# Optimization experiments

Hardware: AMD Instinct MI355X
Metric: run time of the kernel (lower is better)

The kernel has to match this reference:

```python
import math
import jax, jax.numpy as jnp
import numpy as np

NUM_FRAMES = 512
NUM_ANIMALS = 4
N_HEAD = 8
N_EMBD = 512
B = 2
T = NUM_FRAMES * NUM_ANIMALS  # 2048


def _block_causal_mask():
    # tril over frames, full attention within each frame across animals
    tril = jnp.tril(jnp.ones((NUM_FRAMES, NUM_FRAMES), dtype=jnp.float32))
    return jnp.kron(tril, jnp.ones((NUM_ANIMALS, NUM_ANIMALS), dtype=jnp.float32))  # [T, T]


def setup_inputs() -> dict:
    key = jax.random.key(0)
    ks = jax.random.split(key, 6)
    s = 1.0 / math.sqrt(N_EMBD)
    return {
        "x": jax.random.normal(ks[0], (B, T, N_EMBD), dtype=jnp.float32),
        "mask": jnp.ones((B, T), dtype=jnp.int32),
        "Wq": jax.random.normal(ks[1], (N_EMBD, N_EMBD), dtype=jnp.float32) * s,
        "bq": jnp.zeros((N_EMBD,), dtype=jnp.float32),
        "Wk": jax.random.normal(ks[2], (N_EMBD, N_EMBD), dtype=jnp.float32) * s,
        "bk": jnp.zeros((N_EMBD,), dtype=jnp.float32),
        "Wv": jax.random.normal(ks[3], (N_EMBD, N_EMBD), dtype=jnp.float32) * s,
        "bv": jnp.zeros((N_EMBD,), dtype=jnp.float32),
        "Wp": jax.random.normal(ks[4], (N_EMBD, N_EMBD), dtype=jnp.float32) * s,
        "bp": jnp.zeros((N_EMBD,), dtype=jnp.float32),
    }


def reference(x, mask, Wq, bq, Wk, bk, Wv, bv, Wp, bp):
    b, t, c = x.shape
    h, d = N_HEAD, c // N_HEAD
    scale = 1.0 / math.sqrt(d)

    def heads(w, bias):
        return (x @ w + bias).reshape(b, t, h, d).transpose(0, 2, 1, 3)  # [B,H,T,D]

    q = heads(Wq, bq)
    k = heads(Wk, bk)
    v = heads(Wv, bv)

    att = jnp.einsum("bhqd,bhkd->bhqk", q, k) * scale  # [B,H,T,T]
    block = _block_causal_mask()  # [T,T]
    allowed = block[None, None, :, :] * mask[:, None, None, :].astype(jnp.float32)
    att = jnp.where(allowed == 0, -jnp.inf, att)
    att = jax.nn.softmax(att, axis=-1)
    # attn_pdrop = resid_pdrop = 0.0 -> dropout is identity
    y = jnp.einsum("bhqk,bhkd->bhqd", att, v)  # [B,H,T,D]
    y = y.transpose(0, 2, 1, 3).reshape(b, t, c)
    return y @ Wp + bp
```

## Files before the change

kernel.cpp:

```cpp
#include <hip/hip_runtime.h>


typedef unsigned short u16;
typedef unsigned int   u32;
typedef __bf16 bf16x8 __attribute__((ext_vector_type(8)));
typedef float  f32x4  __attribute__((ext_vector_type(4)));
typedef short  s16x4  __attribute__((ext_vector_type(4)));

#define WAITV(n) asm volatile("s_waitcnt vmcnt(" #n ")" ::: "memory")
#define BARRIER() asm volatile("s_barrier" ::: "memory")

static __device__ __forceinline__ u16 f2b(float f) {
  __bf16 h = (__bf16)f;
  return __builtin_bit_cast(u16, h);
}
static __device__ __forceinline__ u32 pack2(float a, float b) {
  return (u32)f2b(a) | ((u32)f2b(b) << 16);
}
static __device__ __forceinline__ bf16x8 ld_bf16x8(const u16* p) {
  uint4 u = *(const uint4*)p;
  return __builtin_bit_cast(bf16x8, u);
}
static __device__ __forceinline__ f32x4 mfma32(bf16x8 a, bf16x8 b, f32x4 c) {
  return __builtin_amdgcn_mfma_f32_16x16x32_bf16(a, b, c, 0, 0, 0);
}
static __device__ __forceinline__ f32x4 mfma16(s16x4 a, s16x4 b, f32x4 c) {
  return __builtin_amdgcn_mfma_f32_16x16x16bf16_1k(a, b, c, 0, 0, 0);
}
static __device__ __forceinline__ void gload16(const u16* g, u16* l) {
  __builtin_amdgcn_global_load_lds(
      (const __attribute__((address_space(1))) void*)g,
      (__attribute__((address_space(3))) void*)l, 16, 0, 0);
}

__global__ __launch_bounds__(256) void k_cvt_x(const float* __restrict__ x,
                                               u16* __restrict__ xb) {
  int i = blockIdx.x * 256 + threadIdx.x;
  const float4* s = (const float4*)x;
  float4 a = s[2 * i], b = s[2 * i + 1];
  uint4 o;
  o.x = pack2(a.x, a.y);
  o.y = pack2(a.z, a.w);
  o.z = pack2(b.x, b.y);
  o.w = pack2(b.z, b.w);
  ((uint4*)xb)[i] = o;
}

__global__ __launch_bounds__(256) void k_cvt_w(
    const float* __restrict__ Wq, const float* __restrict__ Wk,
    const float* __restrict__ Wv, const float* __restrict__ Wp,
    u16* __restrict__ oq, u16* __restrict__ ok,
    u16* __restrict__ ov, u16* __restrict__ op) {
  const int z = blockIdx.z;
  const float* src = (z == 0) ? Wq : (z == 1) ? Wk : (z == 2) ? Wv : Wp;
  u16* dst = (z == 0) ? oq : (z == 1) ? ok : (z == 2) ? ov : op;
  __shared__ float t[32][33];
  const int tx = threadIdx.x, ty = threadIdx.y;
  const int n0 = blockIdx.x * 32, k0 = blockIdx.y * 32;
#pragma unroll
  for (int i = 0; i < 4; ++i)
    t[ty + i * 8][tx] = src[(size_t)(k0 + ty + i * 8) * 512 + n0 + tx];
  __syncthreads();
#pragma unroll
  for (int i = 0; i < 4; ++i)
    dst[(size_t)(n0 + ty + i * 8) * 512 + k0 + tx] = f2b(t[tx][ty + i * 8]);
}

template <int BM, int BN>
__global__ __launch_bounds__(512, 4) void k_gemm(
    const u16* __restrict__ A,
    const u16* __restrict__ Bt_0, const u16* __restrict__ Bt_1,
    const u16* __restrict__ Bt_2,
    const float* __restrict__ bias_0, const float* __restrict__ bias_1,
    const float* __restrict__ bias_2,
    float scl_0, float scl_1, float scl_2,
    void* out_0, void* out_1, void* out_2,
    int mode_0, int mode_1, int mode_2) {
  const int z = blockIdx.z;
  const u16* Bt = (z == 0) ? Bt_0 : (z == 1) ? Bt_1 : Bt_2;
  const float* bias = (z == 0) ? bias_0 : (z == 1) ? bias_1 : bias_2;
  const float scl = (z == 0) ? scl_0 : (z == 1) ? scl_1 : scl_2;
  void* outp = (z == 0) ? out_0 : (z == 1) ? out_1 : out_2;
  const int mode = (z == 0) ? mode_0 : (z == 1) ? mode_1 : mode_2;

  constexpr int MI = BM / 32, NI = BN / 64;
  const int tid = threadIdx.x, lane = tid & 63, w = tid >> 6;
  const int wm = w >> 2, wn = w & 3;
  const int lr = lane & 15, lg = lane >> 4;
  const int m0 = blockIdx.y * BM, n0 = blockIdx.x * BN;

  __shared__ __align__(16) u16 As[3][BM * 64];
  __shared__ __align__(16) u16 Bs[3][BN * 64];

  f32x4 acc[MI][NI];
  const f32x4 fz = {0.f, 0.f, 0.f, 0.f};
#pragma unroll
  for (int mi = 0; mi < MI; ++mi)
#pragma unroll
    for (int ni = 0; ni < NI; ++ni) acc[mi][ni] = fz;

  const int lro = lane >> 3;
  const int lch = (lane & 7) ^ (lro & 7);

  auto stage = [&](int kk, int buf) {
#pragma unroll
    for (int j = 0; j < BM / 64; ++j) {
      const int r0 = w * (BM / 8) + j * 8;
      gload16(A + (size_t)(m0 + r0 + lro) * 512 + kk + lch * 8,
              &As[buf][r0 * 64]);
    }
#pragma unroll
    for (int j = 0; j < BN / 64; ++j) {
      const int r0 = w * (BN / 8) + j * 8;
      gload16(Bt + (size_t)(n0 + r0 + lro) * 512 + kk + lch * 8,
              &Bs[buf][r0 * 64]);
    }
  };

  stage(0, 0);
  stage(64, 1);
  int cur = 0, nx2 = 2;
  for (int kt = 0; kt < 8; ++kt) {
    if (kt < 7) {
      if constexpr (BM / 64 + BN / 64 == 3) WAITV(3); else WAITV(2);
    } else {
      WAITV(0);
    }
    BARRIER();
    if (kt + 2 < 8) stage((kt + 2) * 64, nx2);

#pragma unroll
    for (int kc = 0; kc < 2; ++kc) {
      bf16x8 af[MI], bfv[NI];
#pragma unroll
      for (int mi = 0; mi < MI; ++mi) {
        const int r = wm * (BM / 2) + mi * 16 + lr;
        af[mi] = ld_bf16x8(&As[cur][r * 64 + (((kc * 4 + lg) ^ (r & 7)) << 3)]);
      }
#pragma unroll
      for (int ni = 0; ni < NI; ++ni) {
        const int r = (wn * NI + ni) * 16 + lr;
        bfv[ni] = ld_bf16x8(&Bs[cur][r * 64 + (((kc * 4 + lg) ^ (r & 7)) << 3)]);
      }
#pragma unroll
      for (int mi = 0; mi < MI; ++mi)
#pragma unroll
        for (int ni = 0; ni < NI; ++ni)
          acc[mi][ni] = mfma32(af[mi], bfv[ni], acc[mi][ni]);
    }
    cur = (cur == 2) ? 0 : cur + 1;
    nx2 = (nx2 == 2) ? 0 : nx2 + 1;
  }

#pragma unroll
  for (int mi = 0; mi < MI; ++mi) {
#pragma unroll
    for (int ni = 0; ni < NI; ++ni) {
      const int mbase = m0 + wm * (BM / 2) + mi * 16 + lg * 4;
      const int n = n0 + (wn * NI + ni) * 16 + lr;
      const float bsv = bias[n];
      if (mode == 0) {
        u16* o = (u16*)outp;
#pragma unroll
        for (int i = 0; i < 4; ++i)
          o[(size_t)(mbase + i) * 512 + n] = f2b((acc[mi][ni][i] + bsv) * scl);
      } else if (mode == 1) {
        u16* o = (u16*)outp;
        const int bb = mbase >> 11, t = mbase & 2047;
        const size_t rowb = ((size_t)(bb * 8 + (n >> 6)) * 64 + (n & 63)) * 2048;
        *(u32*)(o + rowb + t)     = pack2(acc[mi][ni][0] + bsv, acc[mi][ni][1] + bsv);
        *(u32*)(o + rowb + t + 2) = pack2(acc[mi][ni][2] + bsv, acc[mi][ni][3] + bsv);
      } else {
        float* o = (float*)outp;
#pragma unroll
        for (int i = 0; i < 4; ++i)
          o[(size_t)(mbase + i) * 512 + n] = acc[mi][ni][i] + bsv;
      }
    }
  }
}

__global__ __launch_bounds__(256, 3) void k_attn(
    const u16* __restrict__ Q, const u16* __restrict__ K,
    const u16* __restrict__ Vt, const int* __restrict__ mask,
    u16* __restrict__ y) {
  const int b = blockIdx.z, h = blockIdx.y;
  const int qt = 31 - blockIdx.x;
  const int tid = threadIdx.x, lane = tid & 63, w = tid >> 6;
  const int lr = lane & 15, lg = lane >> 4;
  const int q0 = qt * 64 + w * 16;
  const int fq = (q0 + lr) >> 2;
  const float NINF = -__builtin_inff();

  __shared__ __align__(16) u16 Ks[3][64 * 64];
  __shared__ __align__(16) u16 Vs[3][64 * 64];

  const size_t brow = (size_t)b * 2048;
  const u16* qp = Q + (brow + q0 + lr) * 512 + h * 64 + lg * 8;
  const bf16x8 qf0 = ld_bf16x8(qp);
  const bf16x8 qf1 = ld_bf16x8(qp + 32);
  const int* maskp = mask + b * 2048;

  const f32x4 fz = {0.f, 0.f, 0.f, 0.f};
  f32x4 yacc[4];
#pragma unroll
  for (int dt = 0; dt < 4; ++dt) yacc[dt] = fz;
  float mrun = NINF, lrun = 0.f;

  const int lro = lane >> 3;
  const int lch = (lane & 7) ^ (lro & 7);
  const u16* kgbase = K + brow * 512 + h * 64 + lch * 8;
  const u16* vgbase = Vt + ((size_t)(b * 8 + h) * 64) * 2048 + lch * 8;

  auto stage = [&](int c, int buf) {
    const int c0 = c << 6;
#pragma unroll
    for (int j = 0; j < 2; ++j) {
      const int r0 = w * 16 + j * 8;
      gload16(kgbase + (size_t)(c0 + r0 + lro) * 512, &Ks[buf][r0 * 64]);
    }
#pragma unroll
    for (int j = 0; j < 2; ++j) {
      const int r0 = w * 16 + j * 8;
      gload16(vgbase + (size_t)(r0 + lro) * 2048 + c0, &Vs[buf][r0 * 64]);
    }
  };

  auto compute = [&](int c, int buf) {
    const int c0 = c << 6;
    int4 mv4[4];
#pragma unroll
    for (int kt = 0; kt < 4; ++kt)
      mv4[kt] = *(const int4*)&maskp[c0 + kt * 16 + lg * 4];

    f32x4 s[4];
#pragma unroll
    for (int kt = 0; kt < 4; ++kt) {
      const int r = kt * 16 + lr;
      s[kt] = mfma32(ld_bf16x8(&Ks[buf][r * 64 + ((lg ^ (r & 7)) << 3)]), qf0, fz);
    }
#pragma unroll
    for (int kt = 0; kt < 4; ++kt) {
      const int r = kt * 16 + lr;
      s[kt] = mfma32(ld_bf16x8(&Ks[buf][r * 64 + (((lg + 4) ^ (r & 7)) << 3)]),
                     qf1, s[kt]);
    }

    float sv[4][4];
    float tm = NINF;
#pragma unroll
    for (int kt = 0; kt < 4; ++kt) {
      const int k0 = c0 + kt * 16;
      const bool kill = ((k0 >> 2) + lg) > fq;
      const int4 mv = mv4[kt];
#pragma unroll
      for (int i = 0; i < 4; ++i) {
        const int mvi = (i == 0) ? mv.x : (i == 1) ? mv.y : (i == 2) ? mv.z : mv.w;
        float v = s[kt][i];
        if (kill || mvi == 0) v = NINF;
        sv[kt][i] = v;
        tm = fmaxf(tm, v);
      }
    }
    tm = fmaxf(tm, __shfl_xor(tm, 16));
    tm = fmaxf(tm, __shfl_xor(tm, 32));

    if (__any(tm > mrun + 8.f)) {
      const float mnew = fmaxf(mrun, tm);
      const float alpha = (mrun == NINF) ? 0.f : exp2f(mrun - mnew);
      lrun *= alpha;
#pragma unroll
      for (int dt = 0; dt < 4; ++dt)
#pragma unroll
        for (int i = 0; i < 4; ++i) yacc[dt][i] *= alpha;
      mrun = mnew;
    }
    const float msafe = (mrun == NINF) ? 0.f : mrun;

    float psum = 0.f;
    s16x4 pf[4];
#pragma unroll
    for (int kt = 0; kt < 4; ++kt) {
#pragma unroll
      for (int i = 0; i < 4; ++i) {
        const float pv = exp2f(sv[kt][i] - msafe);
        psum += pv;
        pf[kt][i] = (short)f2b(pv);
      }
    }
    psum += __shfl_xor(psum, 16);
    psum += __shfl_xor(psum, 32);
    lrun += psum;

#pragma unroll
    for (int dt = 0; dt < 4; ++dt) {
#pragma unroll
      for (int kt = 0; kt < 4; ++kt) {
        const int r = dt * 16 + lr;
        const int ch = kt * 2 + (lg >> 1);
        const uint2 vv = *(const uint2*)&Vs[buf][r * 64 +
                                                 ((ch ^ (r & 7)) << 3) +
                                                 ((lg & 1) << 2)];
        yacc[dt] = mfma16(__builtin_bit_cast(s16x4, vv), pf[kt], yacc[dt]);
      }
    }
  };

  const int nchunk = qt + 1;
  stage(0, 0);
  if (nchunk > 1) stage(1, 1);
  int cur = 0, nx2 = 2;
  for (int c = 0; c < nchunk; ++c) {
    if (c + 1 < nchunk) WAITV(4); else WAITV(0);
    BARRIER();
    if (c + 2 < nchunk) stage(c + 2, nx2);
    compute(c, cur);
    cur = (cur == 2) ? 0 : cur + 1;
    nx2 = (nx2 == 2) ? 0 : nx2 + 1;
  }

  const float inv = 1.f / lrun;
#pragma unroll
  for (int dt = 0; dt < 4; ++dt) {
    u32* p2 = (u32*)(y + (brow + q0 + lr) * 512 + h * 64 + dt * 16 + lg * 4);
    p2[0] = pack2(yacc[dt][0] * inv, yacc[dt][1] * inv);
    p2[1] = pack2(yacc[dt][2] * inv, yacc[dt][3] * inv);
  }
}

extern "C" void kernel_launch(void* const* d_in, const int* in_sizes, int n_in,
                              void* d_out, int out_size, void* d_ws,
                              size_t ws_size, hipStream_t stream) {
  const float* x  = (const float*)d_in[0];
  const int* mask = (const int*)d_in[1];
  const float* Wq = (const float*)d_in[2];
  const float* bq = (const float*)d_in[3];
  const float* Wk = (const float*)d_in[4];
  const float* bk = (const float*)d_in[5];
  const float* Wv = (const float*)d_in[6];
  const float* bv = (const float*)d_in[7];
  const float* Wp = (const float*)d_in[8];
  const float* bp = (const float*)d_in[9];

  char* ws = (char*)d_ws;
  u16* xb  = (u16*)(ws);
  u16* wqt = (u16*)(ws + (4u << 20));
  u16* wkt = (u16*)(ws + (4u << 20) + 524288u);
  u16* wvt = (u16*)(ws + (5u << 20));
  u16* wpt = (u16*)(ws + (5u << 20) + 524288u);
  u16* Qb  = (u16*)(ws + (6u << 20));
  u16* Kb  = (u16*)(ws + (10u << 20));
  u16* Vtb = (u16*)(ws + (14u << 20));
  u16* yb  = (u16*)(ws + (18u << 20));

  const float SCLQ = 0.125f * 1.4426950408889634f;

  k_cvt_x<<<dim3(1024), dim3(256), 0, stream>>>(x, xb);
  k_cvt_w<<<dim3(16, 16, 4), dim3(32, 8), 0, stream>>>(Wq, Wk, Wv, Wp, wqt, wkt,
                                                       wvt, wpt);
  k_gemm<128, 64><<<dim3(8, 32, 3), dim3(512), 0, stream>>>(
      xb, wqt, wkt, wvt, bq, bk, bv, SCLQ, 1.f, 1.f,
      (void*)Qb, (void*)Kb, (void*)Vtb, 0, 0, 1);
  k_attn<<<dim3(32, 8, 2), dim3(256), 0, stream>>>(Qb, Kb, Vtb, mask, yb);
  k_gemm<64, 64><<<dim3(8, 64, 1), dim3(512), 0, stream>>>(
      yb, wpt, wpt, wpt, bp, bp, bp, 1.f, 1.f, 1.f,
      d_out, d_out, d_out, 2, 2, 2);
}
```

Measured before the change: 164.4 us.

## Specialize diagonal attention chunk, preload additive mask to LDS, retile GEMM warps

The attention kernel now peels the diagonal chunk so that only that chunk applies the causal test. It also converts the padding mask into an additive float bias held in LDS, and uses raw v_exp_f32 with a finite initial max. Row-sum reductions are deferred to the end, and LDS address offsets are precomputed. The GEMM is de-templated to a fixed 128x64 tile with a 4x2 warp layout and 32x32 per-warp tiles, and the output projection now uses 128-row tiles. Occupancy hint for attention drops from 3 to 2 blocks because of the extra 8KB of LDS. The finite initial max could misbehave if a whole row is masked.

```diff
diff --git a/kernel.cpp b/kernel.cpp
--- a/kernel.cpp
+++ b/kernel.cpp
@@ -26,6 +26,11 @@
 }
 static __device__ __forceinline__ f32x4 mfma16(s16x4 a, s16x4 b, f32x4 c) {
   return __builtin_amdgcn_mfma_f32_16x16x16bf16_1k(a, b, c, 0, 0, 0);
+}
+static __device__ __forceinline__ float exp2n(float x) {
+  float r;
+  asm("v_exp_f32 %0, %1" : "=v"(r) : "v"(x));
+  return r;
 }
 static __device__ __forceinline__ void gload16(const u16* g, u16* l) {
   __builtin_amdgcn_global_load_lds(
@@ -66,7 +71,6 @@
     dst[(size_t)(n0 + ty + i * 8) * 512 + k0 + tx] = f2b(t[tx][ty + i * 8]);
 }
 
-template <int BM, int BN>
 __global__ __launch_bounds__(512, 4) void k_gemm(
     const u16* __restrict__ A,
     const u16* __restrict__ Bt_0, const u16* __restrict__ Bt_1,
@@ -83,69 +87,65 @@
   void* outp = (z == 0) ? out_0 : (z == 1) ? out_1 : out_2;
   const int mode = (z == 0) ? mode_0 : (z == 1) ? mode_1 : mode_2;
 
-  constexpr int MI = BM / 32, NI = BN / 64;
   const int tid = threadIdx.x, lane = tid & 63, w = tid >> 6;
-  const int wm = w >> 2, wn = w & 3;
+  const int wm = w >> 1, wn = w & 1;
   const int lr = lane & 15, lg = lane >> 4;
-  const int m0 = blockIdx.y * BM, n0 = blockIdx.x * BN;
-
-  __shared__ __align__(16) u16 As[3][BM * 64];
-  __shared__ __align__(16) u16 Bs[3][BN * 64];
-
-  f32x4 acc[MI][NI];
+  const int m0 = blockIdx.y * 128, n0 = blockIdx.x * 64;
+
+  __shared__ __align__(16) u16 As[3][128 * 64];
+  __shared__ __align__(16) u16 Bs[3][64 * 64];
+
+  f32x4 acc[2][2];
   const f32x4 fz = {0.f, 0.f, 0.f, 0.f};
 #pragma unroll
-  for (int mi = 0; mi < MI; ++mi)
-#pragma unroll
-    for (int ni = 0; ni < NI; ++ni) acc[mi][ni] = fz;
+  for (int mi = 0; mi < 2; ++mi)
+#pragma unroll
+    for (int ni = 0; ni < 2; ++ni) acc[mi][ni] = fz;
 
   const int lro = lane >> 3;
   const int lch = (lane & 7) ^ (lro & 7);
 
   auto stage = [&](int kk, int buf) {
 #pragma unroll
-    for (int j = 0; j < BM / 64; ++j) {
-      const int r0 = w * (BM / 8) + j * 8;
+    for (int j = 0; j < 2; ++j) {
+      const int r0 = w * 16 + j * 8;
       gload16(A + (size_t)(m0 + r0 + lro) * 512 + kk + lch * 8,
               &As[buf][r0 * 64]);
     }
-#pragma unroll
-    for (int j = 0; j < BN / 64; ++j) {
-      const int r0 = w * (BN / 8) + j * 8;
+    {
+      const int r0 = w * 8;
       gload16(Bt + (size_t)(n0 + r0 + lro) * 512 + kk + lch * 8,
               &Bs[buf][r0 * 64]);
     }
   };
+
+  const int e0 = ((lg ^ (lr & 7)) << 3);
+  const int e1 = (((4 + lg) ^ (lr & 7)) << 3);
+  const int arow = wm * 32 + lr;
+  const int brow = wn * 32 + lr;
 
   stage(0, 0);
   stage(64, 1);
   int cur = 0, nx2 = 2;
   for (int kt = 0; kt < 8; ++kt) {
-    if (kt < 7) {
-      if constexpr (BM / 64 + BN / 64 == 3) WAITV(3); else WAITV(2);
-    } else {
-      WAITV(0);
-    }
+    if (kt < 7) WAITV(3); else WAITV(0);
     BARRIER();
     if (kt + 2 < 8) stage((kt + 2) * 64, nx2);
 
 #pragma unroll
     for (int kc = 0; kc < 2; ++kc) {
-      bf16x8 af[MI], bfv[NI];
-#pragma unroll
-      for (int mi = 0; mi < MI; ++mi) {
-        const int r = wm * (BM / 2) + mi * 16 + lr;
-        af[mi] = ld_bf16x8(&As[cur][r * 64 + (((kc * 4 + lg) ^ (r & 7)) << 3)]);
-      }
-#pragma unroll
-      for (int ni = 0; ni < NI; ++ni) {
-        const int r = (wn * NI + ni) * 16 + lr;
-        bfv[ni] = ld_bf16x8(&Bs[cur][r * 64 + (((kc * 4 + lg) ^ (r & 7)) << 3)]);
-      }
-#pragma unroll
-      for (int mi = 0; mi < MI; ++mi)
-#pragma unroll
-        for (int ni = 0; ni < NI; ++ni)
+      const int e = (kc == 0) ? e0 : e1;
+      const u16* Ap = &As[cur][arow * 64 + e];
+      const u16* Bp = &Bs[cur][brow * 64 + e];
+      bf16x8 af[2], bfv[2];
+#pragma unroll
+      for (int mi = 0; mi < 2; ++mi) af[mi] = ld_bf16x8(Ap + mi * 1024);
+#pragma unroll
+      for (int ni = 0; ni < 2; ++ni) bfv[ni] = ld_bf16x8(Bp + ni * 1024);
+#pragma unroll
+      for (int mi = 0; mi < 2; ++mi)
+#pragma unroll
+        for (int ni = 0; ni < 2; ++ni)
           acc[mi][ni] = mfma32(af[mi], bfv[ni], acc[mi][ni]);
     }
     cur = (cur == 2) ? 0 : cur + 1;
@@ -153,11 +153,11 @@
   }
 
 #pragma unroll
-  for (int mi = 0; mi < MI; ++mi) {
-#pragma unroll
-    for (int ni = 0; ni < NI; ++ni) {
-      const int mbase = m0 + wm * (BM / 2) + mi * 16 + lg * 4;
-      const int n = n0 + (wn * NI + ni) * 16 + lr;
+  for (int mi = 0; mi < 2; ++mi) {
+#pragma unroll
+    for (int ni = 0; ni < 2; ++ni) {
+      const int mbase = m0 + wm * 32 + mi * 16 + lg * 4;
+      const int n = n0 + wn * 32 + ni * 16 + lr;
       const float bsv = bias[n];
       if (mode == 0) {
         u16* o = (u16*)outp;
@@ -180,7 +180,7 @@
   }
 }
 
-__global__ __launch_bounds__(256, 3) void k_attn(
+__global__ __launch_bounds__(256, 2) void k_attn(
     const u16* __restrict__ Q, const u16* __restrict__ K,
     const u16* __restrict__ Vt, const int* __restrict__ mask,
     u16* __restrict__ y) {
@@ -194,18 +194,29 @@
 
   __shared__ __align__(16) u16 Ks[3][64 * 64];
   __shared__ __align__(16) u16 Vs[3][64 * 64];
+  __shared__ __align__(16) float mb[2048];
+
+  {
+    const int4* m4 = (const int4*)(mask + b * 2048);
+    int4 a = m4[tid * 2], c = m4[tid * 2 + 1];
+    float* d = &mb[tid * 8];
+    d[0] = a.x ? 0.f : NINF; d[1] = a.y ? 0.f : NINF;
+    d[2] = a.z ? 0.f : NINF; d[3] = a.w ? 0.f : NINF;
+    d[4] = c.x ? 0.f : NINF; d[5] = c.y ? 0.f : NINF;
+    d[6] = c.z ? 0.f : NINF; d[7] = c.w ? 0.f : NINF;
+  }
+  __syncthreads();
 
   const size_t brow = (size_t)b * 2048;
   const u16* qp = Q + (brow + q0 + lr) * 512 + h * 64 + lg * 8;
   const bf16x8 qf0 = ld_bf16x8(qp);
   const bf16x8 qf1 = ld_bf16x8(qp + 32);
-  const int* maskp = mask + b * 2048;
 
   const f32x4 fz = {0.f, 0.f, 0.f, 0.f};
   f32x4 yacc[4];
 #pragma unroll
   for (int dt = 0; dt < 4; ++dt) yacc[dt] = fz;
-  float mrun = NINF, lrun = 0.f;
+  float mrun = -1.0e4f, lpart = 0.f;
 
   const int lro = lane >> 3;
   const int lch = (lane & 7) ^ (lro & 7);
@@ -226,100 +237,94 @@
     }
   };
 
-  auto compute = [&](int c, int buf) {
-    const int c0 = c << 6;
-    int4 mv4[4];
+  const int kb0 = lr * 64 + ((lg ^ (lr & 7)) << 3);
+  const int kb1 = lr * 64 + (((4 + lg) ^ (lr & 7)) << 3);
+  const int vf = (lg >> 1) ^ (lr & 7);
+  int vh[4];
+#pragma unroll
+  for (int kt = 0; kt < 4; ++kt)
+    vh[kt] = lr * 64 + (((2 * kt) ^ vf) << 3) + ((lg & 1) << 2);
+
+  auto step = [&](int c, int buf, bool diag) {
+    const u16* kp = &Ks[buf][0];
+    const u16* vp = &Vs[buf][0];
+    const float* mbp = &mb[c * 64 + lg * 4];
+
+    f32x4 s[4];
 #pragma unroll
     for (int kt = 0; kt < 4; ++kt)
-      mv4[kt] = *(const int4*)&maskp[c0 + kt * 16 + lg * 4];
-
-    f32x4 s[4];
-#pragma unroll
-    for (int kt = 0; kt < 4; ++kt) {
-      const int r = kt * 16 + lr;
-      s[kt] = mfma32(ld_bf16x8(&Ks[buf][r * 64 + ((lg ^ (r & 7)) << 3)]), qf0, fz);
-    }
-#pragma unroll
-    for (int kt = 0; kt < 4; ++kt) {
-      const int r = kt * 16 + lr;
-      s[kt] = mfma32(ld_bf16x8(&Ks[buf][r * 64 + (((lg + 4) ^ (r & 7)) << 3)]),
-                     qf1, s[kt]);
-    }
+      s[kt] = mfma32(ld_bf16x8(kp + kb0 + kt * 1024), qf0, fz);
+#pragma unroll
+    for (int kt = 0; kt < 4; ++kt)
+      s[kt] = mfma32(ld_bf16x8(kp + kb1 + kt * 1024), qf1, s[kt]);
 
     float sv[4][4];
     float tm = NINF;
 #pragma unroll
     for (int kt = 0; kt < 4; ++kt) {
-      const int k0 = c0 + kt * 16;
-      const bool kill = ((k0 >> 2) + lg) > fq;
-      const int4 mv = mv4[kt];
+      const float4 mv = *(const float4*)(mbp + kt * 16);
+      float kv = 0.f;
+      if (diag) kv = ((qt * 16 + kt * 4 + lg) > fq) ? NINF : 0.f;
 #pragma unroll
       for (int i = 0; i < 4; ++i) {
-        const int mvi = (i == 0) ? mv.x : (i == 1) ? mv.y : (i == 2) ? mv.z : mv.w;
-        float v = s[kt][i];
-        if (kill || mvi == 0) v = NINF;
-        sv[kt][i] = v;
-        tm = fmaxf(tm, v);
+        const float bi = (i == 0) ? mv.x : (i == 1) ? mv.y : (i == 2) ? mv.z : mv.w;
+        sv[kt][i] = s[kt][i] + bi + kv;
+        tm = fmaxf(tm, sv[kt][i]);
       }
     }
-    tm = fmaxf(tm, __shfl_xor(tm, 16));
-    tm = fmaxf(tm, __shfl_xor(tm, 32));
 
     if (__any(tm > mrun + 8.f)) {
-      const float mnew = fmaxf(mrun, tm);
-      const float alpha = (mrun == NINF) ? 0.f : exp2f(mrun - mnew);
-      lrun *= alpha;
+      float tmr = fmaxf(tm, __shfl_xor(tm, 16));
+      tmr = fmaxf(tmr, __shfl_xor(tmr, 32));
+      const float mnew = fmaxf(mrun, tmr);
+      const float alpha = exp2n(mrun - mnew);
+      lpart *= alpha;
 #pragma unroll
       for (int dt = 0; dt < 4; ++dt)
 #pragma unroll
         for (int i = 0; i < 4; ++i) yacc[dt][i] *= alpha;
       mrun = mnew;
     }
-    const float msafe = (mrun == NINF) ? 0.f : mrun;
-
-    float psum = 0.f;
+
     s16x4 pf[4];
 #pragma unroll
     for (int kt = 0; kt < 4; ++kt) {
 #pragma unroll
       for (int i = 0; i < 4; ++i) {
-        const float pv = exp2f(sv[kt][i] - msafe);
-        psum += pv;
+        const float pv = exp2n(sv[kt][i] - mrun);
+        lpart += pv;
         pf[kt][i] = (short)f2b(pv);
       }
     }
-    psum += __shfl_xor(psum, 16);
-    psum += __shfl_xor(psum, 32);
-    lrun += psum;
 
 #pragma unroll
     for (int dt = 0; dt < 4; ++dt) {
 #pragma unroll
       for (int kt = 0; kt < 4; ++kt) {
-        const int r = dt * 16 + lr;
-        const int ch = kt * 2 + (lg >> 1);
-        const uint2 vv = *(const uint2*)&Vs[buf][r * 64 +
-                                                 ((ch ^ (r & 7)) << 3) +
-                                                 ((lg & 1) << 2)];
+        const uint2 vv = *(const uint2*)(vp + vh[kt] + dt * 1024);
         yacc[dt] = mfma16(__builtin_bit_cast(s16x4, vv), pf[kt], yacc[dt]);
       }
     }
   };
 
-  const int nchunk = qt + 1;
   stage(0, 0);
-  if (nchunk > 1) stage(1, 1);
+  if (qt > 0) stage(1, 1);
   int cur = 0, nx2 = 2;
-  for (int c = 0; c < nchunk; ++c) {
-    if (c + 1 < nchunk) WAITV(4); else WAITV(0);
+  for (int c = 0; c < qt; ++c) {
+    WAITV(4);
     BARRIER();
-    if (c + 2 < nchunk) stage(c + 2, nx2);
-    compute(c, cur);
+    if (c + 2 <= qt) stage(c + 2, nx2);
+    step(c, cur, false);
     cur = (cur == 2) ? 0 : cur + 1;
     nx2 = (nx2 == 2) ? 0 : nx2 + 1;
   }
-
-  const float inv = 1.f / lrun;
+  WAITV(0);
+  BARRIER();
+  step(qt, cur, true);
+
+  float lsum = lpart + __shfl_xor(lpart, 16);
+  lsum += __shfl_xor(lsum, 32);
+  const float inv = 1.f / lsum;
 #pragma unroll
   for (int dt = 0; dt < 4; ++dt) {
     u32* p2 = (u32*)(y + (brow + q0 + lr) * 512 + h * 64 + dt * 16 + lg * 4);
@@ -358,11 +363,11 @@
   k_cvt_x<<<dim3(1024), dim3(256), 0, stream>>>(x, xb);
   k_cvt_w<<<dim3(16, 16, 4), dim3(32, 8), 0, stream>>>(Wq, Wk, Wv, Wp, wqt, wkt,
                                                        wvt, wpt);
-  k_gemm<128, 64><<<dim3(8, 32, 3), dim3(512), 0, stream>>>(
+  k_gemm<<<dim3(8, 32, 3), dim3(512), 0, stream>>>(
       xb, wqt, wkt, wvt, bq, bk, bv, SCLQ, 1.f, 1.f,
       (void*)Qb, (void*)Kb, (void*)Vtb, 0, 0, 1);
   k_attn<<<dim3(32, 8, 2), dim3(256), 0, stream>>>(Qb, Kb, Vtb, mask, yb);
-  k_gemm<64, 64><<<dim3(8, 64, 1), dim3(512), 0, stream>>>(
+  k_gemm<<<dim3(8, 32, 1), dim3(512), 0, stream>>>(
       yb, wpt, wpt, wpt, bp, bp, bp, 1.f, 1.f, 1.f,
       d_out, d_out, d_out, 2, 2, 2);
 }
```

Result: faster. 148.1 us (-9.9%).
